# Kernel tuning notes

Measured on AMD Instinct MI355X. Metric: run time of the kernel, lower is better.

The kernel has to match this reference:

```python
import jax, jax.numpy as jnp
import numpy as np

D_MODEL = 256
MLP_DIM = 1024
EPS = 1e-5

def _layernorm(x, g, b):
    mu = jnp.mean(x, axis=-1, keepdims=True)
    var = jnp.mean(jnp.square(x - mu), axis=-1, keepdims=True)
    return (x - mu) * jax.lax.rsqrt(var + EPS) * g + b

def setup_inputs() -> dict:
    key = jax.random.key(0)
    ks = jax.random.split(key, 4)
    d, m = D_MODEL, MLP_DIM
    x = jax.random.normal(ks[0], (8, 1024, 4, d), dtype=jnp.float32)
    w_qkv = jax.random.normal(ks[1], (3 * d, d), dtype=jnp.float32) * 0.05  # torch Linear weight (out,in)
    gamma1 = jnp.ones((d,), jnp.float32)
    beta1 = jnp.zeros((d,), jnp.float32)
    gamma2 = jnp.ones((d,), jnp.float32)
    beta2 = jnp.zeros((d,), jnp.float32)
    w1 = jax.random.normal(ks[2], (m, d), dtype=jnp.float32) * 0.05
    b1 = jnp.zeros((m,), jnp.float32)
    w2 = jax.random.normal(ks[3], (d, m), dtype=jnp.float32) * 0.05
    b2 = jnp.zeros((d,), jnp.float32)
    return {"x": x, "w_qkv": w_qkv, "gamma1": gamma1, "beta1": beta1,
            "gamma2": gamma2, "beta2": beta2, "w1": w1, "b1": b1, "w2": w2, "b2": b2}

def reference(x, w_qkv, gamma1, beta1, gamma2, beta2, w1, b1, w2, b2):
    bsz, n, h, d = x.shape
    scale = d ** -0.5
    # --- attention branch: x + attn(norm1(x)) ---
    xn = _layernorm(x, gamma1, beta1)
    # Linear(d, 3d): xn @ W^T, then reshape trailing 3d -> (d, 3) as in torch
    qkv = jnp.einsum('bnhd,ed->bnhe', xn, w_qkv).reshape(bsz, n * h, d, 3)
    q, k, v = qkv[..., 0], qkv[..., 1], qkv[..., 2]   # [b, n*h, d]
    dots = jnp.einsum('bid,bjd->bij', q, k) * scale   # [b, n*h, n*h]
    attn = jax.nn.softmax(dots, axis=-1)              # dropout=0 -> identity
    out = jnp.einsum('bij,bjd->bid', attn, v).reshape(bsz, n, h, d)
    x = x + out
    # --- mlp branch: x + mlp(norm2(x)) ---
    xn2 = _layernorm(x, gamma2, beta2)
    hid = jax.nn.silu(jnp.einsum('bnhd,md->bnhm', xn2, w1) + b1)
    x = x + jnp.einsum('bnhm,dm->bnhd', hid, w2) + b2
    return x
```

## Files before the change

kernel.cpp:

```cpp
#include <hip/hip_runtime.h>


typedef __attribute__((ext_vector_type(8))) short bf16x8;
typedef __attribute__((ext_vector_type(4))) short bf16x4;
typedef __attribute__((ext_vector_type(4))) float f32x4;
typedef __attribute__((ext_vector_type(16))) float f32x16;

static __device__ __forceinline__ short f2bf(float f) {
    union { float f; unsigned u; } v; v.f = f;
    unsigned r = (v.u + 0x7FFFu + ((v.u >> 16) & 1u)) >> 16;
    return (short)r;
}

static __device__ __forceinline__ void gll16(const void* g, void* l) {
    __builtin_amdgcn_global_load_lds(
        (const __attribute__((address_space(1))) unsigned*)g,
        (__attribute__((address_space(3))) unsigned*)l, 16, 0, 0);
}

__global__ __launch_bounds__(256) void k_cvt(const float* __restrict__ wqkv,
                                             const float* __restrict__ w1,
                                             const float* __restrict__ w2,
                                             short* __restrict__ owqkv,
                                             short* __restrict__ ow1,
                                             short* __restrict__ ow2) {
    int i = blockIdx.x * 256 + threadIdx.x;
    if (i < 196608) {
        int e = i >> 8, col = i & 255;
        int dd = e / 3, which = e - dd * 3;
        float v = wqkv[i];
        if (which == 0) v *= 0.0625f * 1.44269504f;
        owqkv[((which << 8) + dd) * 256 + col] = f2bf(v);
    }
    if (i < 262144) { ow1[i] = f2bf(w1[i]); ow2[i] = f2bf(w2[i]); }
}

__global__ __launch_bounds__(256) void k_ln(const float* __restrict__ x,
                                            const float* __restrict__ g,
                                            const float* __restrict__ bta,
                                            short* __restrict__ out) {
    int w = threadIdx.x >> 6, lane = threadIdx.x & 63;
    long row = (long)blockIdx.x * 4 + w;
    float4 v = *((const float4*)(x + row * 256) + lane);
    float s = v.x + v.y + v.z + v.w;
    float q = v.x * v.x + v.y * v.y + v.z * v.z + v.w * v.w;
    for (int off = 1; off < 64; off <<= 1) {
        s += __shfl_xor(s, off);
        q += __shfl_xor(q, off);
    }
    float mean = s * (1.0f / 256.0f);
    float var = q * (1.0f / 256.0f) - mean * mean;
    float rstd = rsqrtf(var + 1e-5f);
    float4 gg = *((const float4*)g + lane);
    float4 bb = *((const float4*)bta + lane);
    short4 o;
    o.x = f2bf((v.x - mean) * rstd * gg.x + bb.x);
    o.y = f2bf((v.y - mean) * rstd * gg.y + bb.y);
    o.z = f2bf((v.z - mean) * rstd * gg.z + bb.z);
    o.w = f2bf((v.w - mean) * rstd * gg.w + bb.w);
    *((short4*)(out + row * 256) + lane) = o;
}

__global__ __launch_bounds__(256) void k_qkv(const short* __restrict__ xn,
                                             const short* __restrict__ wb,
                                             short* __restrict__ Q,
                                             short* __restrict__ K,
                                             short* __restrict__ VT) {
    __shared__ __attribute__((aligned(16))) short lds_a[64 * 264];
    __shared__ __attribute__((aligned(16))) short lds_b[64 * 264];
    int t = threadIdx.x;
    int m0 = blockIdx.y * 64, n0 = blockIdx.x * 64;
    const int4* ga = (const int4*)xn;
    const int4* gb = (const int4*)wb;
    int4* la = (int4*)lds_a;
    int4* lb = (int4*)lds_b;
    for (int it = 0; it < 8; it++) {
        int c = t + 256 * it;
        int r = c >> 5, k = c & 31;
        la[r * 33 + k] = ga[(long)(m0 + r) * 32 + k];
        lb[r * 33 + k] = gb[(n0 + r) * 32 + k];
    }
    __syncthreads();
    int w = t >> 6, lane = t & 63, ln = lane & 15, qd = lane >> 4;
    int moff = (w >> 1) * 32, noff = (w & 1) * 32;
    f32x4 acc[2][2] = {};
    for (int ks = 0; ks < 8; ks++) {
        bf16x8 a0 = *(const bf16x8*)&lds_a[(moff + ln) * 264 + ks * 32 + qd * 8];
        bf16x8 a1 = *(const bf16x8*)&lds_a[(moff + 16 + ln) * 264 + ks * 32 + qd * 8];
        bf16x8 b0 = *(const bf16x8*)&lds_b[(noff + ln) * 264 + ks * 32 + qd * 8];
        bf16x8 b1 = *(const bf16x8*)&lds_b[(noff + 16 + ln) * 264 + ks * 32 + qd * 8];
        acc[0][0] = __builtin_amdgcn_mfma_f32_16x16x32_bf16(a0, b0, acc[0][0], 0, 0, 0);
        acc[0][1] = __builtin_amdgcn_mfma_f32_16x16x32_bf16(a0, b1, acc[0][1], 0, 0, 0);
        acc[1][0] = __builtin_amdgcn_mfma_f32_16x16x32_bf16(a1, b0, acc[1][0], 0, 0, 0);
        acc[1][1] = __builtin_amdgcn_mfma_f32_16x16x32_bf16(a1, b1, acc[1][1], 0, 0, 0);
    }
    for (int mi = 0; mi < 2; mi++)
        for (int nj = 0; nj < 2; nj++)
            for (int rg = 0; rg < 4; rg++) {
                float v = acc[mi][nj][rg];
                int gr = m0 + moff + mi * 16 + qd * 4 + rg;
                int e = n0 + noff + nj * 16 + ln;
                int which = e >> 8, dd = e & 255;
                short bv = f2bf(v);
                if (which == 0) Q[(long)gr * 256 + dd] = bv;
                else if (which == 1) K[(long)gr * 256 + dd] = bv;
                else {
                    int b = gr >> 12, i = gr & 4095;
                    VT[((long)b * 256 + dd) * 4096 + i] = bv;
                }
            }
}

__global__ __launch_bounds__(512, 2) void k_attn(const short* __restrict__ Q,
                                                 const short* __restrict__ K,
                                                 const short* __restrict__ VT,
                                                 const float* __restrict__ x,
                                                 float* __restrict__ out) {
    __shared__ __attribute__((aligned(16))) short lds_k[2][64 * 256];
    __shared__ __attribute__((aligned(16))) short lds_v[2][2][256 * 40];
    int t = threadIdx.x, w = t >> 6, l = t & 63, l5 = l & 31, h = l >> 5;
    int ww = w & 3, hkv = w >> 2;
    int b = blockIdx.x;
    int q0 = blockIdx.y * 128 + ww * 32;

    bf16x8 qf[16];
    {
        const short* qrow = Q + ((long)(b * 4096 + q0 + l5)) * 256;
        #pragma unroll
        for (int kc = 0; kc < 16; kc++) qf[kc] = *(const bf16x8*)(qrow + kc * 16 + h * 8);
    }
    f32x16 O[8] = {};
    float lsum = 0.f;

    const char* Kb = (const char*)(K + (long)b * 4096 * 256);
    const int4* gv = (const int4*)(VT + (long)b * 4096 * 256);

    int koff[4], klds[4];
    #pragma unroll
    for (int i = 0; i < 4; i++) {
        int r = w * 8 + i * 2 + (l >> 5);
        koff[i] = r * 512 + ((l5 ^ (r & 31)) * 16);
        klds[i] = (w * 8 + i * 2) * 512;
    }
    int vgbase[4], vloff[4];
    #pragma unroll
    for (int i = 0; i < 4; i++) {
        int c = t + 512 * i;
        int sub = c >> 10, cc = c & 1023, d = cc >> 2, ch = cc & 3;
        vgbase[i] = d * 512 + sub * 4 + ch;
        vloff[i] = sub * 20480 + d * 80 + ch * 16;
    }
    int4 vs[4];

    #pragma unroll
    for (int i = 0; i < 4; i++) vs[i] = gv[vgbase[i]];
    #pragma unroll
    for (int i = 0; i < 4; i++) gll16(Kb + koff[i], (char*)lds_k[0] + klds[i]);
    #pragma unroll
    for (int i = 0; i < 4; i++)
        *(int4*)((char*)lds_v + vloff[i]) = vs[i];
    __syncthreads();

    const char* lvmine = (const char*)lds_v + hkv * 20480;

    for (int jt = 0; jt < 64; jt++) {
        int cur = jt & 1;
        if (jt < 63) {
            #pragma unroll
            for (int i = 0; i < 4; i++) vs[i] = gv[vgbase[i] + (jt + 1) * 8];
            int ka = (jt + 1) * 32768;
            #pragma unroll
            for (int i = 0; i < 4; i++)
                gll16(Kb + ka + koff[i], (char*)lds_k[cur ^ 1] + klds[i]);
        }
        const short* lk = lds_k[cur] + hkv * 32 * 256;
        const char* lv = lvmine + cur * 40960;
        f32x16 st = {};
        #pragma unroll
        for (int kc = 0; kc < 16; kc++) {
            int cc = kc * 2 + h;
            bf16x8 a = *(const bf16x8*)(lk + (l5 * 32 + (cc ^ l5)) * 8);
            st = __builtin_amdgcn_mfma_f32_32x32x16_bf16(a, qf[kc], st, 0, 0, 0);
        }
        unsigned pw[4][2];
        #pragma unroll
        for (int r4 = 0; r4 < 4; r4++) {
            float p0 = __builtin_amdgcn_exp2f(st[r4 * 4 + 0]);
            float p1 = __builtin_amdgcn_exp2f(st[r4 * 4 + 1]);
            float p2 = __builtin_amdgcn_exp2f(st[r4 * 4 + 2]);
            float p3 = __builtin_amdgcn_exp2f(st[r4 * 4 + 3]);
            lsum += (p0 + p1) + (p2 + p3);
            union { float f; unsigned u; } u0, u1, u2, u3;
            u0.f = p0; u1.f = p1; u2.f = p2; u3.f = p3;
            pw[r4][0] = __builtin_amdgcn_perm(u1.u + 0x8000u, u0.u + 0x8000u, 0x07060302u);
            pw[r4][1] = __builtin_amdgcn_perm(u3.u + 0x8000u, u2.u + 0x8000u, 0x07060302u);
        }
        bf16x8 pfr[2];
        #pragma unroll
        for (int k2 = 0; k2 < 2; k2++) {
            unsigned a0 = pw[2 * k2][0], a1 = pw[2 * k2][1];
            unsigned b0 = pw[2 * k2 + 1][0], b1 = pw[2 * k2 + 1][1];
            asm("v_permlane32_swap_b32 %0, %1" : "+v"(a0), "+v"(b0));
            asm("v_permlane32_swap_b32 %0, %1" : "+v"(a1), "+v"(b1));
            union { unsigned u[4]; bf16x8 v; } f;
            f.u[0] = a0; f.u[1] = a1; f.u[2] = b0; f.u[3] = b1;
            pfr[k2] = f.v;
        }
        if (jt < 63) {
            #pragma unroll
            for (int i = 0; i < 4; i++)
                *(int4*)((char*)lds_v + (cur ^ 1) * 40960 + vloff[i]) = vs[i];
        }
        #pragma unroll
        for (int dt = 0; dt < 8; dt++) {
            const char* vbase = lv + (dt * 32 + l5) * 80;
            #pragma unroll
            for (int k2 = 0; k2 < 2; k2++) {
                bf16x8 va = *(const bf16x8*)(vbase + (k2 * 2 + h) * 16);
                O[dt] = __builtin_amdgcn_mfma_f32_32x32x16_bf16(va, pfr[k2], O[dt], 0, 0, 0);
            }
        }
        __syncthreads();
    }

    float lt = lsum + __shfl_xor(lsum, 32);
    float* lmrg = (float*)&lds_v[1][0][0];
    lmrg[hkv * 128 + ww * 32 + l5] = lt;
    __syncthreads();
    float ltot = lmrg[ww * 32 + l5] + lmrg[128 + ww * 32 + l5];
    float rinv = 1.0f / ltot;

    float* omrg = (float*)&lds_v[0][0][0];
    float* fscr = (float*)lds_k[0] + ww * (32 * 33);
    #pragma unroll
    for (int dt = 0; dt < 8; dt++) {
        if (hkv == 1) {
            #pragma unroll
            for (int r = 0; r < 16; r++) omrg[ww * 1024 + r * 64 + l] = O[dt][r];
        }
        __syncthreads();
        if (hkv == 0) {
            #pragma unroll
            for (int r = 0; r < 16; r++) {
                float Om = O[dt][r] + omrg[ww * 1024 + r * 64 + l];
                int drow = (r & 3) + 8 * (r >> 2) + 4 * h;
                fscr[drow * 33 + l5] = Om * rinv;
            }
            asm volatile("s_waitcnt lgkmcnt(0)" ::: "memory");
            #pragma unroll
            for (int it = 0; it < 16; it++) {
                int ql = it * 2 + h;
                float v = fscr[l5 * 33 + ql];
                long idx = ((long)(b * 4096 + q0 + ql)) * 256 + dt * 32 + l5;
                out[idx] = x[idx] + v;
            }
            asm volatile("s_waitcnt lgkmcnt(0)" ::: "memory");
        }
        __syncthreads();
    }
}

__global__ __launch_bounds__(256) void k_mlp(const short* __restrict__ xn,
                                             const short* __restrict__ w1b,
                                             const short* __restrict__ w2b,
                                             const float* __restrict__ b1,
                                             const float* __restrict__ b2,
                                             float* __restrict__ out) {
    __shared__ __attribute__((aligned(16))) short lds_w[2][16 * 256];
    __shared__ __attribute__((aligned(16))) short lds_h[4][16 * 264];
    int t = threadIdx.x, w = t >> 6, l = t & 63, ln = l & 15, qd = l >> 4;
    int R0 = blockIdx.x * 64 + w * 16;
    short* lhs = lds_h[w];

    bf16x8 a1f[8];
    #pragma unroll
    for (int kc = 0; kc < 8; kc++)
        a1f[kc] = *(const bf16x8*)(xn + (long)(R0 + ln) * 256 + kc * 32 + qd * 8);

    int rr[2]; long s1off[2], s2off[2]; int wlds[2];
    #pragma unroll
    for (int i = 0; i < 2; i++) {
        int r = w * 4 + i * 2 + (l >> 5);
        int ch = (l & 31) ^ r;
        rr[i] = r;
        s1off[i] = (long)r * 512 + ch * 16;
        s2off[i] = (long)r * 2048 + ch * 16;
        wlds[i] = (w * 4 + i * 2) * 512;
    }
    const char* W1c = (const char*)w1b;
    const char* W2c = (const char*)w2b;

    f32x4 Oc[16] = {};
    #pragma unroll
    for (int i = 0; i < 2; i++)
        gll16(W1c + s1off[i], (char*)lds_w[0] + wlds[i]);
    __syncthreads();
    int cur = 0;

    for (int pass = 0; pass < 4; pass++) {
        for (int nt = 0; nt < 16; nt++) {
            if (nt < 15) {
                long base = (long)(pass * 256 + (nt + 1) * 16) * 512;
                #pragma unroll
                for (int i = 0; i < 2; i++)
                    gll16(W1c + base + s1off[i], (char*)lds_w[cur ^ 1] + wlds[i]);
            } else {
                long base = (long)pass * 512;
                #pragma unroll
                for (int i = 0; i < 2; i++)
                    gll16(W2c + base + s2off[i], (char*)lds_w[cur ^ 1] + wlds[i]);
            }
            f32x4 acc = {};
            const short* lw = lds_w[cur];
            #pragma unroll
            for (int kc = 0; kc < 8; kc++) {
                int cc = kc * 4 + qd;
                bf16x8 bf = *(const bf16x8*)(lw + (ln * 32 + (cc ^ ln)) * 8);
                acc = __builtin_amdgcn_mfma_f32_16x16x32_bf16(a1f[kc], bf, acc, 0, 0, 0);
            }
            float bb = b1[pass * 256 + nt * 16 + ln];
            #pragma unroll
            for (int rg = 0; rg < 4; rg++) {
                float z = acc[rg] + bb;
                float sv = z / (1.0f + __expf(-z));
                lhs[(qd * 4 + rg) * 264 + nt * 16 + ln] = f2bf(sv);
            }
            __syncthreads();
            cur ^= 1;
        }
        bf16x8 a2f[8];
        #pragma unroll
        for (int kc = 0; kc < 8; kc++)
            a2f[kc] = *(const bf16x8*)&lhs[ln * 264 + kc * 32 + qd * 8];
        for (int nt = 0; nt < 16; nt++) {
            if (nt < 15) {
                long base = (long)((nt + 1) * 16) * 2048 + (long)pass * 512;
                #pragma unroll
                for (int i = 0; i < 2; i++)
                    gll16(W2c + base + s2off[i], (char*)lds_w[cur ^ 1] + wlds[i]);
            } else if (pass < 3) {
                long base = (long)((pass + 1) * 256) * 512;
                #pragma unroll
                for (int i = 0; i < 2; i++)
                    gll16(W1c + base + s1off[i], (char*)lds_w[cur ^ 1] + wlds[i]);
            }
            const short* lw = lds_w[cur];
            #pragma unroll
            for (int kc = 0; kc < 8; kc++) {
                int cc = kc * 4 + qd;
                bf16x8 bf = *(const bf16x8*)(lw + (ln * 32 + (cc ^ ln)) * 8);
                Oc[nt] = __builtin_amdgcn_mfma_f32_16x16x32_bf16(a2f[kc], bf, Oc[nt], 0, 0, 0);
            }
            __syncthreads();
            cur ^= 1;
        }
    }
    for (int nt = 0; nt < 16; nt++) {
        int dd = nt * 16 + ln;
        float bb = b2[dd];
        #pragma unroll
        for (int rg = 0; rg < 4; rg++) {
            long idx = (long)(R0 + qd * 4 + rg) * 256 + dd;
            out[idx] = out[idx] + Oc[nt][rg] + bb;
        }
    }
}

extern "C" void kernel_launch(void* const* d_in, const int* in_sizes, int n_in,
                              void* d_out, int out_size, void* d_ws, size_t ws_size,
                              hipStream_t stream) {
    const float* x    = (const float*)d_in[0];
    const float* wqkv = (const float*)d_in[1];
    const float* g1   = (const float*)d_in[2];
    const float* be1  = (const float*)d_in[3];
    const float* g2   = (const float*)d_in[4];
    const float* be2  = (const float*)d_in[5];
    const float* w1   = (const float*)d_in[6];
    const float* b1   = (const float*)d_in[7];
    const float* w2   = (const float*)d_in[8];
    const float* b2   = (const float*)d_in[9];
    float* out = (float*)d_out;
    char* ws = (char*)d_ws;
    short* WQKV = (short*)(ws);
    short* W1B  = (short*)(ws + (512l << 10));
    short* W2B  = (short*)(ws + (1l << 20));
    short* XN   = (short*)(ws + (2l << 20));
    short* Qb   = (short*)(ws + (18l << 20));
    short* Kb   = (short*)(ws + (34l << 20));
    short* VTb  = (short*)(ws + (50l << 20));

    k_cvt<<<1024, 256, 0, stream>>>(wqkv, w1, w2, WQKV, W1B, W2B);
    k_ln<<<8192, 256, 0, stream>>>(x, g1, be1, XN);
    k_qkv<<<dim3(12, 512), 256, 0, stream>>>(XN, WQKV, Qb, Kb, VTb);
    k_attn<<<dim3(8, 32), 512, 0, stream>>>(Qb, Kb, VTb, x, out);
    k_ln<<<8192, 256, 0, stream>>>(out, g2, be2, XN);
    k_mlp<<<512, 256, 0, stream>>>(XN, W1B, W2B, b1, b2, out);
}
```

Before: 438.0 us.

## Split QK accumulator chains, raise MFMA priority, and double MLP weight tile size

In the attention kernel, the QK^T reduction is split into two independent MFMA accumulator chains that are summed before exp2, which shortens the dependent MFMA chain. s_setprio is raised around the MFMA sections so these waves get issue priority over the others. In the MLP kernel, each LDS weight tile now holds 32 output rows instead of 16, which halves the number of barriers and pipeline steps per pass, and the loops are fully unrolled. The cost is more LDS use, more registers, and larger unrolled code.

After: 490.7 us. 1.12x slower.

```diff
diff --git a/kernel.cpp b/kernel.cpp
--- a/kernel.cpp
+++ b/kernel.cpp
@@ -175,20 +175,24 @@
         }
         const short* lk = lds_k[cur] + hkv * 32 * 256;
         const char* lv = lvmine + cur * 40960;
-        f32x16 st = {};
-        #pragma unroll
-        for (int kc = 0; kc < 16; kc++) {
-            int cc = kc * 2 + h;
-            bf16x8 a = *(const bf16x8*)(lk + (l5 * 32 + (cc ^ l5)) * 8);
-            st = __builtin_amdgcn_mfma_f32_32x32x16_bf16(a, qf[kc], st, 0, 0, 0);
-        }
+        f32x16 st0 = {}, st1 = {};
+        __builtin_amdgcn_s_setprio(1);
+        #pragma unroll
+        for (int kc = 0; kc < 16; kc += 2) {
+            int c0 = kc * 2 + h, c1 = (kc + 1) * 2 + h;
+            bf16x8 a0 = *(const bf16x8*)(lk + (l5 * 32 + (c0 ^ l5)) * 8);
+            bf16x8 a1 = *(const bf16x8*)(lk + (l5 * 32 + (c1 ^ l5)) * 8);
+            st0 = __builtin_amdgcn_mfma_f32_32x32x16_bf16(a0, qf[kc], st0, 0, 0, 0);
+            st1 = __builtin_amdgcn_mfma_f32_32x32x16_bf16(a1, qf[kc + 1], st1, 0, 0, 0);
+        }
+        __builtin_amdgcn_s_setprio(0);
         unsigned pw[4][2];
         #pragma unroll
         for (int r4 = 0; r4 < 4; r4++) {
-            float p0 = __builtin_amdgcn_exp2f(st[r4 * 4 + 0]);
-            float p1 = __builtin_amdgcn_exp2f(st[r4 * 4 + 1]);
-            float p2 = __builtin_amdgcn_exp2f(st[r4 * 4 + 2]);
-            float p3 = __builtin_amdgcn_exp2f(st[r4 * 4 + 3]);
+            float p0 = __builtin_amdgcn_exp2f(st0[r4 * 4 + 0] + st1[r4 * 4 + 0]);
+            float p1 = __builtin_amdgcn_exp2f(st0[r4 * 4 + 1] + st1[r4 * 4 + 1]);
+            float p2 = __builtin_amdgcn_exp2f(st0[r4 * 4 + 2] + st1[r4 * 4 + 2]);
+            float p3 = __builtin_amdgcn_exp2f(st0[r4 * 4 + 3] + st1[r4 * 4 + 3]);
             lsum += (p0 + p1) + (p2 + p3);
             union { float f; unsigned u; } u0, u1, u2, u3;
             u0.f = p0; u1.f = p1; u2.f = p2; u3.f = p3;
@@ -211,6 +215,7 @@
             for (int i = 0; i < 4; i++)
                 *(int4*)((char*)lds_v + (cur ^ 1) * 40960 + vloff[i]) = vs[i];
         }
+        __builtin_amdgcn_s_setprio(1);
         #pragma unroll
         for (int dt = 0; dt < 8; dt++) {
             const char* vbase = lv + (dt * 32 + l5) * 80;
@@ -220,6 +225,7 @@
                 O[dt] = __builtin_amdgcn_mfma_f32_32x32x16_bf16(va, pfr[k2], O[dt], 0, 0, 0);
             }
         }
+        __builtin_amdgcn_s_setprio(0);
         __syncthreads();
     }
 
@@ -266,9 +272,9 @@
                                              const float* __restrict__ b1,
                                              const float* __restrict__ b2,
                                              float* __restrict__ out) {
-    __shared__ __attribute__((aligned(16))) short lds_w[2][16 * 256];
+    __shared__ __attribute__((aligned(16))) short lds_w[2][32 * 256];
     __shared__ __attribute__((aligned(16))) short lds_h[4][16 * 264];
-    int t = threadIdx.x, w = t >> 6, l = t & 63, ln = l & 15, qd = l >> 4;
+    int t = threadIdx.x, w = t >> 6, l = t & 63, l5 = l & 31, ln = l & 15, qd = l >> 4;
     int R0 = blockIdx.x * 64 + w * 16;
     short* lhs = lds_h[w];
 
@@ -277,53 +283,57 @@
     for (int kc = 0; kc < 8; kc++)
         a1f[kc] = *(const bf16x8*)(xn + (long)(R0 + ln) * 256 + kc * 32 + qd * 8);
 
-    int rr[2]; long s1off[2], s2off[2]; int wlds[2];
-    #pragma unroll
-    for (int i = 0; i < 2; i++) {
-        int r = w * 4 + i * 2 + (l >> 5);
-        int ch = (l & 31) ^ r;
-        rr[i] = r;
+    long s1off[4], s2off[4]; int wlds[4];
+    #pragma unroll
+    for (int i = 0; i < 4; i++) {
+        int r = w * 8 + i * 2 + (l >> 5);
+        int ch = l5 ^ (r & 31);
         s1off[i] = (long)r * 512 + ch * 16;
         s2off[i] = (long)r * 2048 + ch * 16;
-        wlds[i] = (w * 4 + i * 2) * 512;
+        wlds[i] = (w * 8 + i * 2) * 512;
     }
     const char* W1c = (const char*)w1b;
     const char* W2c = (const char*)w2b;
 
-    f32x4 Oc[16] = {};
-    #pragma unroll
-    for (int i = 0; i < 2; i++)
+    f32x4 Oc[8][2] = {};
+    #pragma unroll
+    for (int i = 0; i < 4; i++)
         gll16(W1c + s1off[i], (char*)lds_w[0] + wlds[i]);
     __syncthreads();
     int cur = 0;
 
     for (int pass = 0; pass < 4; pass++) {
-        for (int nt = 0; nt < 16; nt++) {
-            if (nt < 15) {
-                long base = (long)(pass * 256 + (nt + 1) * 16) * 512;
-                #pragma unroll
-                for (int i = 0; i < 2; i++)
+        #pragma unroll
+        for (int nt = 0; nt < 8; nt++) {
+            if (nt < 7) {
+                long base = (long)(pass * 256 + (nt + 1) * 32) * 512;
+                #pragma unroll
+                for (int i = 0; i < 4; i++)
                     gll16(W1c + base + s1off[i], (char*)lds_w[cur ^ 1] + wlds[i]);
             } else {
                 long base = (long)pass * 512;
                 #pragma unroll
-                for (int i = 0; i < 2; i++)
+                for (int i = 0; i < 4; i++)
                     gll16(W2c + base + s2off[i], (char*)lds_w[cur ^ 1] + wlds[i]);
             }
-            f32x4 acc = {};
             const short* lw = lds_w[cur];
             #pragma unroll
-            for (int kc = 0; kc < 8; kc++) {
-                int cc = kc * 4 + qd;
-                bf16x8 bf = *(const bf16x8*)(lw + (ln * 32 + (cc ^ ln)) * 8);
-                acc = __builtin_amdgcn_mfma_f32_16x16x32_bf16(a1f[kc], bf, acc, 0, 0, 0);
-            }
-            float bb = b1[pass * 256 + nt * 16 + ln];
-            #pragma unroll
-            for (int rg = 0; rg < 4; rg++) {
-                float z = acc[rg] + bb;
-                float sv = z / (1.0f + __expf(-z));
-                lhs[(qd * 4 + rg) * 264 + nt * 16 + ln] = f2bf(sv);
+            for (int g = 0; g < 2; g++) {
+                int lr = g * 16 + ln;
+                f32x4 acc = {};
+                #pragma unroll
+                for (int kc = 0; kc < 8; kc++) {
+                    int cc = kc * 4 + qd;
+                    bf16x8 bf = *(const bf16x8*)(lw + lr * 256 + (cc ^ lr) * 8);
+                    acc = __builtin_amdgcn_mfma_f32_16x16x32_bf16(a1f[kc], bf, acc, 0, 0, 0);
+                }
+                float bb = b1[pass * 256 + nt * 32 + lr];
+                #pragma unroll
+                for (int rg = 0; rg < 4; rg++) {
+                    float z = acc[rg] + bb;
+                    float sv = z / (1.0f + __expf(-z));
+                    lhs[(qd * 4 + rg) * 264 + nt * 32 + lr] = f2bf(sv);
+                }
             }
             __syncthreads();
             cur ^= 1;
@@ -332,38 +342,46 @@
         #pragma unroll
         for (int kc = 0; kc < 8; kc++)
             a2f[kc] = *(const bf16x8*)&lhs[ln * 264 + kc * 32 + qd * 8];
-        for (int nt = 0; nt < 16; nt++) {
-            if (nt < 15) {
-                long base = (long)((nt + 1) * 16) * 2048 + (long)pass * 512;
-                #pragma unroll
-                for (int i = 0; i < 2; i++)
+        #pragma unroll
+        for (int nt = 0; nt < 8; nt++) {
+            if (nt < 7) {
+                long base = (long)((nt + 1) * 32) * 2048 + (long)pass * 512;
+                #pragma unroll
+                for (int i = 0; i < 4; i++)
                     gll16(W2c + base + s2off[i], (char*)lds_w[cur ^ 1] + wlds[i]);
             } else if (pass < 3) {
                 long base = (long)((pass + 1) * 256) * 512;
                 #pragma unroll
-                for (int i = 0; i < 2; i++)
+                for (int i = 0; i < 4; i++)
                     gll16(W1c + base + s1off[i], (char*)lds_w[cur ^ 1] + wlds[i]);
             }
             const short* lw = lds_w[cur];
             #pragma unroll
-            for (int kc = 0; kc < 8; kc++) {
-                int cc = kc * 4 + qd;
-                bf16x8 bf = *(const bf16x8*)(lw + (ln * 32 + (cc ^ ln)) * 8);
-                Oc[nt] = __builtin_amdgcn_mfma_f32_16x16x32_bf16(a2f[kc], bf, Oc[nt], 0, 0, 0);
+            for (int g = 0; g < 2; g++) {
+                int lr = g * 16 + ln;
+                #pragma unroll
+                for (int kc = 0; kc < 8; kc++) {
+                    int cc = kc * 4 + qd;
+                    bf16x8 bf = *(const bf16x8*)(lw + lr * 256 + (cc ^ lr) * 8);
+                    Oc[nt][g] = __builtin_amdgcn_mfma_f32_16x16x32_bf16(a2f[kc], bf, Oc[nt][g], 0, 0, 0);
+                }
             }
             __syncthreads();
             cur ^= 1;
         }
     }
-    for (int nt = 0; nt < 16; nt++) {
-        int dd = nt * 16 + ln;
-        float bb = b2[dd];
-        #pragma unroll
-        for (int rg = 0; rg < 4; rg++) {
-            long idx = (long)(R0 + qd * 4 + rg) * 256 + dd;
-            out[idx] = out[idx] + Oc[nt][rg] + bb;
-        }
-    }
+    #pragma unroll
+    for (int nt = 0; nt < 8; nt++)
+        #pragma unroll
+        for (int g = 0; g < 2; g++) {
+            int dd = nt * 32 + g * 16 + ln;
+            float bb = b2[dd];
+            #pragma unroll
+            for (int rg = 0; rg < 4; rg++) {
+                long idx = (long)(R0 + qd * 4 + rg) * 256 + dd;
+                out[idx] = out[idx] + Oc[nt][g][rg] + bb;
+            }
+        }
 }
 
 extern "C" void kernel_launch(void* const* d_in, const int* in_sizes, int n_in,
```
